# Kernel tuning notes

Hardware: AMD Instinct MI355X
Metric: run time of the kernel (lower is better)

The kernel has to match this reference:

```python
import jax, jax.numpy as jnp
import numpy as np
from math import sqrt

D_K = 64
HEADS = 16


def setup_inputs() -> dict:
    key = jax.random.key(0)
    k1, k2, k3 = jax.random.split(key, 3)
    B, S, D = 2, 2048, HEADS * D_K
    queries = jax.random.normal(k1, (B, S, D), dtype=jnp.float32)
    keys = jax.random.normal(k2, (B, S, D), dtype=jnp.float32)
    values = jax.random.normal(k3, (B, S, D), dtype=jnp.float32)
    # causal mask: 1 where attention is disallowed (j > i), 0 elsewhere
    mask = jnp.triu(jnp.ones((S, S), dtype=jnp.int32), k=1)[None, None]  # [1,1,S,S]
    return {"queries": queries, "keys": keys, "values": values, "mask": mask}


def reference(queries, keys, values, mask):
    B, S, _ = queries.shape
    # [B, S, H*Dk] -> [B, H, S, Dk]
    def split_heads(x):
        return x.reshape(B, -1, HEADS, D_K).transpose(0, 2, 1, 3)

    q = split_heads(queries)
    k = split_heads(keys)
    v = split_heads(values)
    # scores: [B, H, Sq, Sk]
    attn = jnp.einsum('bhqd,bhkd->bhqk', q, k) / sqrt(D_K)
    attn = attn + mask.astype(attn.dtype) * jnp.asarray(-1e9, attn.dtype)
    w = jax.nn.softmax(attn, axis=-1)
    out = jnp.einsum('bhqk,bhkd->bhqd', w, v)  # [B, H, Sq, Dk]
    return out
```

## Files before the change

kernel.cpp:

```cpp
#include <hip/hip_runtime.h>
#include <hip/hip_bf16.h>

#define S_LEN 2048
#define NH 16
#define DK 64
#define DM 1024
#define QBLK 64
#define KVBLK 64
#define NQT 32
#define KPAD 72

typedef float f32x4 __attribute__((ext_vector_type(4)));
typedef __bf16 bf16x8 __attribute__((ext_vector_type(8)));

__device__ __forceinline__ int vswz(int row) { return ((row >> 3) & 3) << 4; }

__device__ __forceinline__ void kv_issue(const float* __restrict__ kp_t,
                                         const float* __restrict__ vp_t,
                                         int tid, int w, int l,
                                         float4 (&kr)[2][2], float (&vr)[16]) {
#pragma unroll
  for (int it = 0; it < 2; ++it) {
    int f = tid + it * 256;
    int row = f >> 3, cb8 = f & 7;
    const float* src = kp_t + (size_t)row * DM + cb8 * 8;
    kr[it][0] = *reinterpret_cast<const float4*>(src);
    kr[it][1] = *reinterpret_cast<const float4*>(src + 4);
  }
#pragma unroll
  for (int it = 0; it < 4; ++it) {
#pragma unroll
    for (int r = 0; r < 4; ++r)
      vr[it * 4 + r] = vp_t[(size_t)(4 * w + 16 * it + r) * DM + l];
  }
}

__device__ __forceinline__ void kv_write(__bf16* __restrict__ Kb, __bf16* __restrict__ Vb,
                                         int tid, int w, int l,
                                         const float4 (&kr)[2][2], const float (&vr)[16]) {
#pragma unroll
  for (int it = 0; it < 2; ++it) {
    int f = tid + it * 256;
    int row = f >> 3, cb8 = f & 7;
    bf16x8 kb;
    kb[0] = (__bf16)kr[it][0].x; kb[1] = (__bf16)kr[it][0].y;
    kb[2] = (__bf16)kr[it][0].z; kb[3] = (__bf16)kr[it][0].w;
    kb[4] = (__bf16)kr[it][1].x; kb[5] = (__bf16)kr[it][1].y;
    kb[6] = (__bf16)kr[it][1].z; kb[7] = (__bf16)kr[it][1].w;
    *reinterpret_cast<bf16x8*>(&Kb[row * KPAD + cb8 * 8]) = kb;
  }
#pragma unroll
  for (int half = 0; half < 2; ++half) {
    bf16x8 vb;
#pragma unroll
    for (int j = 0; j < 8; ++j) vb[j] = (__bf16)vr[half * 8 + j];
    char* p = reinterpret_cast<char*>(Vb) +
              (((l * KPAD + half * 32 + w * 8) * 2) ^ vswz(l));
    *reinterpret_cast<bf16x8*>(p) = vb;
  }
}

__device__ __forceinline__ void mask_diagT(f32x4 (&s)[4], int kv0, int q0,
                                           int w, int l16, int hi) {
  const int ig = q0 + w * 16 + l16;
#pragma unroll
  for (int n = 0; n < 4; ++n)
#pragma unroll
    for (int r = 0; r < 4; ++r) {
      int jg = kv0 + n * 16 + hi * 4 + r;
      if (jg > ig) s[n][r] = -1e30f;
    }
}

__device__ __forceinline__ float sm_expT(f32x4 (&s)[4]) {
  float a0 = 0.f, a1 = 0.f;
#pragma unroll
  for (int n = 0; n < 4; ++n) {
    float p0 = __builtin_amdgcn_exp2f(s[n][0]);
    float p1 = __builtin_amdgcn_exp2f(s[n][1]);
    float p2 = __builtin_amdgcn_exp2f(s[n][2]);
    float p3 = __builtin_amdgcn_exp2f(s[n][3]);
    s[n][0] = p0; s[n][1] = p1; s[n][2] = p2; s[n][3] = p3;
    a0 += p0 + p1;
    a1 += p2 + p3;
  }
  return a0 + a1;
}

__device__ __forceinline__ void packT(const f32x4 (&s)[4], bf16x8 (&pa)[2]) {
#pragma unroll
  for (int c = 0; c < 2; ++c) {
    bf16x8 a;
#pragma unroll
    for (int j = 0; j < 8; ++j) a[j] = (__bf16)s[2 * c + (j >> 2)][j & 3];
    pa[c] = a;
  }
}

__device__ __forceinline__ void load_q_frags(const float* __restrict__ qp, int q0,
                                             int w, int l16, int hi, bf16x8 (&aq)[2]) {
  const float* qr = qp + (size_t)(q0 + w * 16 + l16) * DM;
  const float qs = 0.125f * 1.44269504089f;
#pragma unroll
  for (int c = 0; c < 2; ++c) {
    float4 f0 = *reinterpret_cast<const float4*>(qr + c * 32 + hi * 8);
    float4 f1 = *reinterpret_cast<const float4*>(qr + c * 32 + hi * 8 + 4);
    bf16x8 a;
    a[0] = (__bf16)(f0.x * qs); a[1] = (__bf16)(f0.y * qs);
    a[2] = (__bf16)(f0.z * qs); a[3] = (__bf16)(f0.w * qs);
    a[4] = (__bf16)(f1.x * qs); a[5] = (__bf16)(f1.y * qs);
    a[6] = (__bf16)(f1.z * qs); a[7] = (__bf16)(f1.w * qs);
    aq[c] = a;
  }
}

__device__ __forceinline__ void store_out(float* __restrict__ Og, int b, int h, int q0,
                                          int w, int l, int l16, int hi,
                                          const f32x4 (&o_acc)[4], float l_chain) {
  float lf = l_chain;
  lf += __shfl_xor(lf, 16);
  lf += __shfl_xor(lf, 32);
  float invl = 1.0f / lf;
  float inv[4];
#pragma unroll
  for (int r = 0; r < 4; ++r)
    inv[r] = __shfl(invl, (l & 48) | (hi * 4 + r));
  float* op = Og + ((size_t)(b * NH + h) * S_LEN + q0 + w * 16) * DK;
#pragma unroll
  for (int n = 0; n < 4; ++n)
#pragma unroll
    for (int r = 0; r < 4; ++r)
      op[(size_t)(hi * 4 + r) * DK + n * 16 + l16] = o_acc[n][r] * inv[r];
}

__global__ __launch_bounds__(256, 2)
void fa_fwd_causal(const float* __restrict__ Qg, const float* __restrict__ Kg,
                   const float* __restrict__ Vg, float* __restrict__ Og) {
  __shared__ __align__(16) __bf16 Kl[2][KVBLK * KPAD];
  __shared__ __align__(16) __bf16 Vt[2][DK * KPAD];

  const int bid  = blockIdx.x;
  const int xcd  = bid & 7;
  const int s    = bid >> 3;
  const int p_raw = s & 15;
  const int bb   = (s >> 4) & 1;
  const int hh   = (s >> 5) & 1;
  const int pair = hh ? (15 - p_raw) : p_raw;
  const int b    = bb;
  const int h    = xcd + 8 * hh;

  const int qta = pair;
  const int qtb = NQT - 1 - pair;
  const int q0a = qta * QBLK;
  const int q0b = qtb * QBLK;

  const int tid = threadIdx.x;
  const int w   = tid >> 6;
  const int l   = tid & 63;
  const int l16 = l & 15;
  const int hi  = l >> 4;

  const size_t base_in = (size_t)b * S_LEN * DM + (size_t)h * DK;
  const float* qp = Qg + base_in;
  const float* kp = Kg + base_in;
  const float* vp = Vg + base_in;

  bf16x8 aqA[2], aqB[2];
  load_q_frags(qp, q0a, w, l16, hi, aqA);
  load_q_frags(qp, q0b, w, l16, hi, aqB);

  f32x4 oA[4], oB[4];
  float lA = 0.f, lB = 0.f;
#pragma unroll
  for (int n = 0; n < 4; ++n) { oA[n] = (f32x4){0.f,0.f,0.f,0.f}; oB[n] = (f32x4){0.f,0.f,0.f,0.f}; }

  float4 kr[2][2];
  float  vr[16];
  kv_issue(kp, vp, tid, w, l, kr, vr);

  int cur = 0;
  const int n_tiles = qtb + 1;
  for (int t = 0; t < n_tiles; ++t) {
    const int kv0 = t * KVBLK;
    kv_write(Kl[cur], Vt[cur], tid, w, l, kr, vr);
    if (t + 1 < n_tiles)
      kv_issue(kp + (size_t)(kv0 + KVBLK) * DM, vp + (size_t)(kv0 + KVBLK) * DM,
               tid, w, l, kr, vr);
    asm volatile("s_waitcnt lgkmcnt(0)" ::: "memory");
    __builtin_amdgcn_s_barrier();
    const __bf16* Kb = Kl[cur];
    const __bf16* Vb = Vt[cur];

    if (t <= qta) {
      f32x4 sA[4], sB[4];
#pragma unroll
      for (int n = 0; n < 4; ++n) { sA[n] = (f32x4){0.f,0.f,0.f,0.f}; sB[n] = (f32x4){0.f,0.f,0.f,0.f}; }
#pragma unroll
      for (int n = 0; n < 4; ++n)
#pragma unroll
        for (int c = 0; c < 2; ++c) {
          bf16x8 kf = *reinterpret_cast<const bf16x8*>(&Kb[(n * 16 + l16) * KPAD + c * 32 + hi * 8]);
          sB[n] = __builtin_amdgcn_mfma_f32_16x16x32_bf16(kf, aqB[c], sB[n], 0, 0, 0);
          sA[n] = __builtin_amdgcn_mfma_f32_16x16x32_bf16(kf, aqA[c], sA[n], 0, 0, 0);
        }
      if (t == qta) mask_diagT(sA, kv0, q0a, w, l16, hi);
      lB += sm_expT(sB);
      lA += sm_expT(sA);
      bf16x8 paA[2], paB[2];
      packT(sB, paB);
      packT(sA, paA);
#pragma unroll
      for (int c = 0; c < 2; ++c)
#pragma unroll
        for (int n = 0; n < 4; ++n) {
          int row = n * 16 + l16;
          const char* vpb = reinterpret_cast<const char*>(Vb) +
                            (((row * KPAD + c * 32 + hi * 8) * 2) ^ vswz(row));
          bf16x8 vf = *reinterpret_cast<const bf16x8*>(vpb);
          oB[n] = __builtin_amdgcn_mfma_f32_16x16x32_bf16(paB[c], vf, oB[n], 0, 0, 0);
          oA[n] = __builtin_amdgcn_mfma_f32_16x16x32_bf16(paA[c], vf, oA[n], 0, 0, 0);
        }
    } else {
      f32x4 sB[4];
#pragma unroll
      for (int n = 0; n < 4; ++n) sB[n] = (f32x4){0.f,0.f,0.f,0.f};
#pragma unroll
      for (int n = 0; n < 4; ++n)
#pragma unroll
        for (int c = 0; c < 2; ++c) {
          bf16x8 kf = *reinterpret_cast<const bf16x8*>(&Kb[(n * 16 + l16) * KPAD + c * 32 + hi * 8]);
          sB[n] = __builtin_amdgcn_mfma_f32_16x16x32_bf16(kf, aqB[c], sB[n], 0, 0, 0);
        }
      if (t == qtb) mask_diagT(sB, kv0, q0b, w, l16, hi);
      lB += sm_expT(sB);
      bf16x8 paB[2];
      packT(sB, paB);
#pragma unroll
      for (int c = 0; c < 2; ++c)
#pragma unroll
        for (int n = 0; n < 4; ++n) {
          int row = n * 16 + l16;
          const char* vpb = reinterpret_cast<const char*>(Vb) +
                            (((row * KPAD + c * 32 + hi * 8) * 2) ^ vswz(row));
          bf16x8 vf = *reinterpret_cast<const bf16x8*>(vpb);
          oB[n] = __builtin_amdgcn_mfma_f32_16x16x32_bf16(paB[c], vf, oB[n], 0, 0, 0);
        }
    }
    cur ^= 1;
  }

  store_out(Og, b, h, q0a, w, l, l16, hi, oA, lA);
  store_out(Og, b, h, q0b, w, l, l16, hi, oB, lB);
}

extern "C" void kernel_launch(void* const* d_in, const int* in_sizes, int n_in,
                              void* d_out, int out_size, void* d_ws, size_t ws_size,
                              hipStream_t stream) {
  const float* q = (const float*)d_in[0];
  const float* k = (const float*)d_in[1];
  const float* v = (const float*)d_in[2];
  float* out = (float*)d_out;
  const int blocks = 2 * NH * (NQT / 2);
  hipLaunchKernelGGL(fa_fwd_causal, dim3(blocks), dim3(256), 0, stream, q, k, v, out);
}
```

Before: 43.54 us.

## Split KV range across two blocks per query pair and combine partials

Each paired-query-tile block's KV loop is split into two halves handled by separate blocks, doubling the grid to 1024 blocks. Unnormalized partial outputs (bf16) and row sums are written to workspace, and a second kernel sums them and normalizes. This targets low occupancy and tail imbalance with only 512 blocks. The cost is an extra launch, workspace traffic, and bf16 rounding of the partial accumulators. It falls back to the paired kernel when the workspace is too small.

```diff
diff --git a/kernel.cpp b/kernel.cpp
--- a/kernel.cpp
+++ b/kernel.cpp
@@ -9,6 +9,9 @@
 #define KVBLK 64
 #define NQT 32
 #define KPAD 72
+
+#define SLOT_BYTES 16896
+#define N_SLOTS 1024
 
 typedef float f32x4 __attribute__((ext_vector_type(4)));
 typedef __bf16 bf16x8 __attribute__((ext_vector_type(8)));
@@ -133,9 +136,194 @@
       op[(size_t)(hi * 4 + r) * DK + n * 16 + l16] = o_acc[n][r] * inv[r];
 }
 
+__device__ __forceinline__ void store_partial(char* wsslot, int sel,
+                                              int w, int l16, int hi,
+                                              const f32x4 (&o_acc)[4], float l_chain) {
+  float lf = l_chain;
+  lf += __shfl_xor(lf, 16);
+  lf += __shfl_xor(lf, 32);
+  __bf16* Wn = reinterpret_cast<__bf16*>(wsslot) + sel * 4096;
+  float*  Wl = reinterpret_cast<float*>(wsslot + 16384) + sel * 64;
+#pragma unroll
+  for (int n = 0; n < 4; ++n)
+#pragma unroll
+    for (int r = 0; r < 4; ++r)
+      Wn[(w * 16 + hi * 4 + r) * 64 + n * 16 + l16] = (__bf16)o_acc[n][r];
+  if (hi == 0) Wl[w * 16 + l16] = lf;
+}
+
+__global__ __launch_bounds__(256, 3)
+void fa_split(const float* __restrict__ Qg, const float* __restrict__ Kg,
+              const float* __restrict__ Vg, char* __restrict__ ws) {
+  __shared__ __align__(16) __bf16 Kl[2][KVBLK * KPAD];
+  __shared__ __align__(16) __bf16 Vt[2][DK * KPAD];
+
+  const int bid = blockIdx.x;
+  const int xcd = bid & 7;
+  const int s   = bid >> 3;
+  const int u   = s & 31;
+  const int p4  = u & 15;
+  const int bb  = (u >> 4) & 1;
+  const int v   = s >> 5;
+  const int kap = v & 1;
+  const int hh  = (v >> 1) & 1;
+  const int p   = hh ? (15 - p4) : p4;
+  const int b   = bb;
+  const int h   = xcd + 8 * hh;
+
+  const int qta = p;
+  const int qtb = NQT - 1 - p;
+  const int q0a = qta * QBLK;
+  const int q0b = qtb * QBLK;
+  const int nt  = qtb + 1;
+  const int s0  = (nt + 1) >> 1;
+  const int t0  = kap ? s0 : 0;
+  const int t1  = kap ? nt : s0;
+
+  const int tid = threadIdx.x;
+  const int w   = tid >> 6;
+  const int l   = tid & 63;
+  const int l16 = l & 15;
+  const int hi  = l >> 4;
+
+  const size_t base_in = (size_t)b * S_LEN * DM + (size_t)h * DK;
+  const float* qp = Qg + base_in;
+  const float* kp = Kg + base_in;
+  const float* vp = Vg + base_in;
+
+  bf16x8 aqA[2], aqB[2];
+  load_q_frags(qp, q0a, w, l16, hi, aqA);
+  load_q_frags(qp, q0b, w, l16, hi, aqB);
+
+  f32x4 oA[4], oB[4];
+  float lA = 0.f, lB = 0.f;
+#pragma unroll
+  for (int n = 0; n < 4; ++n) { oA[n] = (f32x4){0.f,0.f,0.f,0.f}; oB[n] = (f32x4){0.f,0.f,0.f,0.f}; }
+
+  float4 kr[2][2];
+  float  vr[16];
+  kv_issue(kp + (size_t)t0 * KVBLK * DM, vp + (size_t)t0 * KVBLK * DM, tid, w, l, kr, vr);
+
+  int cur = 0;
+  for (int t = t0; t < t1; ++t) {
+    const int kv0 = t * KVBLK;
+    kv_write(Kl[cur], Vt[cur], tid, w, l, kr, vr);
+    if (t + 1 < t1)
+      kv_issue(kp + (size_t)(kv0 + KVBLK) * DM, vp + (size_t)(kv0 + KVBLK) * DM,
+               tid, w, l, kr, vr);
+    asm volatile("s_waitcnt lgkmcnt(0)" ::: "memory");
+    __builtin_amdgcn_s_barrier();
+    const __bf16* Kb = Kl[cur];
+    const __bf16* Vb = Vt[cur];
+
+    if (t <= qta) {
+      f32x4 sA[4], sB[4];
+#pragma unroll
+      for (int n = 0; n < 4; ++n) { sA[n] = (f32x4){0.f,0.f,0.f,0.f}; sB[n] = (f32x4){0.f,0.f,0.f,0.f}; }
+#pragma unroll
+      for (int n = 0; n < 4; ++n)
+#pragma unroll
+        for (int c = 0; c < 2; ++c) {
+          bf16x8 kf = *reinterpret_cast<const bf16x8*>(&Kb[(n * 16 + l16) * KPAD + c * 32 + hi * 8]);
+          sB[n] = __builtin_amdgcn_mfma_f32_16x16x32_bf16(kf, aqB[c], sB[n], 0, 0, 0);
+          sA[n] = __builtin_amdgcn_mfma_f32_16x16x32_bf16(kf, aqA[c], sA[n], 0, 0, 0);
+        }
+      if (t == qta) mask_diagT(sA, kv0, q0a, w, l16, hi);
+      lB += sm_expT(sB);
+      lA += sm_expT(sA);
+      bf16x8 paA[2], paB[2];
+      packT(sB, paB);
+      packT(sA, paA);
+#pragma unroll
+      for (int c = 0; c < 2; ++c)
+#pragma unroll
+        for (int n = 0; n < 4; ++n) {
+          int row = n * 16 + l16;
+          const char* vpb = reinterpret_cast<const char*>(Vb) +
+                            (((row * KPAD + c * 32 + hi * 8) * 2) ^ vswz(row));
+          bf16x8 vf = *reinterpret_cast<const bf16x8*>(vpb);
+          oB[n] = __builtin_amdgcn_mfma_f32_16x16x32_bf16(paB[c], vf, oB[n], 0, 0, 0);
+          oA[n] = __builtin_amdgcn_mfma_f32_16x16x32_bf16(paA[c], vf, oA[n], 0, 0, 0);
+        }
+    } else {
+      f32x4 sB[4];
+#pragma unroll
+      for (int n = 0; n < 4; ++n) sB[n] = (f32x4){0.f,0.f,0.f,0.f};
+#pragma unroll
+      for (int n = 0; n < 4; ++n)
+#pragma unroll
+        for (int c = 0; c < 2; ++c) {
+          bf16x8 kf = *reinterpret_cast<const bf16x8*>(&Kb[(n * 16 + l16) * KPAD + c * 32 + hi * 8]);
+          sB[n] = __builtin_amdgcn_mfma_f32_16x16x32_bf16(kf, aqB[c], sB[n], 0, 0, 0);
+        }
+      if (t == qtb) mask_diagT(sB, kv0, q0b, w, l16, hi);
+      lB += sm_expT(sB);
+      bf16x8 paB[2];
+      packT(sB, paB);
+#pragma unroll
+      for (int c = 0; c < 2; ++c)
+#pragma unroll
+        for (int n = 0; n < 4; ++n) {
+          int row = n * 16 + l16;
+          const char* vpb = reinterpret_cast<const char*>(Vb) +
+                            (((row * KPAD + c * 32 + hi * 8) * 2) ^ vswz(row));
+          bf16x8 vf = *reinterpret_cast<const bf16x8*>(vpb);
+          oB[n] = __builtin_amdgcn_mfma_f32_16x16x32_bf16(paB[c], vf, oB[n], 0, 0, 0);
+        }
+    }
+    cur ^= 1;
+  }
+
+  char* slot = ws + (size_t)((((b * NH + h) * 16 + p) * 2 + kap)) * SLOT_BYTES;
+  store_partial(slot, 0, w, l16, hi, oA, lA);
+  store_partial(slot, 1, w, l16, hi, oB, lB);
+}
+
+__global__ __launch_bounds__(256, 8)
+void fa_combine(const char* __restrict__ ws, float* __restrict__ Og) {
+  const int bid = blockIdx.x;
+  const int qt  = bid & 31;
+  const int h   = (bid >> 5) & 15;
+  const int b   = bid >> 9;
+  const int p   = (qt < 16) ? qt : (31 - qt);
+  const int sel = (qt < 16) ? 0 : 1;
+
+  const char* slot0 = ws + (size_t)(((b * NH + h) * 16 + p) * 2 + 0) * SLOT_BYTES;
+  const char* slot1 = slot0 + SLOT_BYTES;
+  const __bf16* N0 = reinterpret_cast<const __bf16*>(slot0) + sel * 4096;
+  const __bf16* N1 = reinterpret_cast<const __bf16*>(slot1) + sel * 4096;
+  const float*  L0 = reinterpret_cast<const float*>(slot0 + 16384) + sel * 64;
+  const float*  L1 = reinterpret_cast<const float*>(slot1 + 16384) + sel * 64;
+
+  const int t   = threadIdx.x;
+  const int row = t >> 2;
+  const int cq  = t & 3;
+  const float inv = 1.0f / (L0[row] + L1[row]);
+
+  float* op = Og + ((size_t)(b * NH + h) * S_LEN + qt * QBLK + row) * DK + cq * 16;
+  const __bf16* a0 = N0 + row * 64 + cq * 16;
+  const __bf16* a1 = N1 + row * 64 + cq * 16;
+#pragma unroll
+  for (int k = 0; k < 2; ++k) {
+    bf16x8 x0 = *reinterpret_cast<const bf16x8*>(a0 + k * 8);
+    bf16x8 x1 = *reinterpret_cast<const bf16x8*>(a1 + k * 8);
+    float4 o0, o1;
+    o0.x = ((float)x0[0] + (float)x1[0]) * inv;
+    o0.y = ((float)x0[1] + (float)x1[1]) * inv;
+    o0.z = ((float)x0[2] + (float)x1[2]) * inv;
+    o0.w = ((float)x0[3] + (float)x1[3]) * inv;
+    o1.x = ((float)x0[4] + (float)x1[4]) * inv;
+    o1.y = ((float)x0[5] + (float)x1[5]) * inv;
+    o1.z = ((float)x0[6] + (float)x1[6]) * inv;
+    o1.w = ((float)x0[7] + (float)x1[7]) * inv;
+    *reinterpret_cast<float4*>(op + k * 8)     = o0;
+    *reinterpret_cast<float4*>(op + k * 8 + 4) = o1;
+  }
+}
+
 __global__ __launch_bounds__(256, 2)
-void fa_fwd_causal(const float* __restrict__ Qg, const float* __restrict__ Kg,
-                   const float* __restrict__ Vg, float* __restrict__ Og) {
+void fa_paired(const float* __restrict__ Qg, const float* __restrict__ Kg,
+               const float* __restrict__ Vg, float* __restrict__ Og) {
   __shared__ __align__(16) __bf16 Kl[2][KVBLK * KPAD];
   __shared__ __align__(16) __bf16 Vt[2][DK * KPAD];
 
@@ -260,6 +448,11 @@
   const float* k = (const float*)d_in[1];
   const float* v = (const float*)d_in[2];
   float* out = (float*)d_out;
-  const int blocks = 2 * NH * (NQT / 2);
-  hipLaunchKernelGGL(fa_fwd_causal, dim3(blocks), dim3(256), 0, stream, q, k, v, out);
-}
+  const size_t need = (size_t)N_SLOTS * SLOT_BYTES;
+  if (ws_size >= need) {
+    hipLaunchKernelGGL(fa_split, dim3(1024), dim3(256), 0, stream, q, k, v, (char*)d_ws);
+    hipLaunchKernelGGL(fa_combine, dim3(1024), dim3(256), 0, stream, (const char*)d_ws, out);
+  } else {
+    hipLaunchKernelGGL(fa_paired, dim3(512), dim3(256), 0, stream, q, k, v, out);
+  }
+}
```

New measurement: 79.41 us. 82.4% more time.
